# Performance work log

Hardware: AMD Instinct MI355X
Metric: run time of the kernel (lower is better)

The kernel has to match this reference:

```python
import jax, jax.numpy as jnp
import numpy as np

CONV_DIMS = (-3, -2)   # spatial dims (channel-last layout)
RADIUS = (3, 3)        # window = 1 + 2*r = 7 per dim -> 49 cells
STEP = (1, 1)


def _unfold(x, dim, window, step):
    """torch.Tensor.unfold: dim -> out_len, window appended as last axis."""
    dim = dim % x.ndim
    n = x.shape[dim]
    starts = jnp.arange((n - window) // step + 1) * step          # [L]
    idx = starts[:, None] + jnp.arange(window)[None, :]           # [L, w]
    y = jnp.take(x, idx, axis=dim)                                # dim -> [L, w]
    return jnp.moveaxis(y, dim + 1, -1)                           # window axis to last


def _local_attention(x):
    # Unfold each conv dim; move its window axis to the front (as in the torch code).
    for i, r, s in zip(CONV_DIMS, RADIUS, STEP):
        x = _unfold(x, i, 1 + 2 * r, s)
        x = jnp.moveaxis(x, -1, 0)
    n_win = len(CONV_DIMS)
    cells = int(np.prod(x.shape[:n_win]))
    x = x.reshape((cells,) + x.shape[n_win:])      # [cells, B, H', W', C]
    center = cells // 2                            # spatial center of the window
    q = jnp.moveaxis(x[center:center + 1], 0, -2)  # [B, H', W', 1, C]
    k = jnp.moveaxis(jnp.concatenate([x[:center], x[center + 1:]], axis=0), 0, -2)  # [B,H',W',cells-1,C]
    d = q.shape[-1]
    scores = jnp.einsum('...qc,...kc->...qk', q, k) / jnp.sqrt(jnp.asarray(d, q.dtype))
    w = jax.nn.softmax(scores, axis=-1)
    out = jnp.einsum('...qk,...kc->...qc', w, k)   # keys double as values
    return out.squeeze(-2)                          # [B, H', W', C]


def setup_inputs() -> dict:
    key = jax.random.key(0)
    X = jax.random.normal(key, (4, 64, 64, 256), dtype=jnp.float32)
    return {"X": X}


def reference(X):
    return _local_attention(X)
```

## Files before the change

### kernel.cpp

```cpp
#include <hip/hip_runtime.h>

#define B_   4
#define H_   64
#define W_   64
#define C_   256
#define HO_  58
#define WO_  58
#define TI_  29
#define TJ_  8
#define GRID (B_ * TI_ * TJ_)

typedef __attribute__((ext_vector_type(8))) short bf16x8;
typedef __attribute__((ext_vector_type(4))) float f32x4;

__device__ __forceinline__ void split2(float a, float b, unsigned& hi, unsigned& lo) {
    unsigned ua = __builtin_bit_cast(unsigned, a);
    unsigned ub = __builtin_bit_cast(unsigned, b);
    hi = (ua >> 16) | (ub & 0xFFFF0000u);
    float ra = a - __builtin_bit_cast(float, ua & 0xFFFF0000u);
    float rb = b - __builtin_bit_cast(float, ub & 0xFFFF0000u);
    lo = (__builtin_bit_cast(unsigned, ra) >> 16) |
         (__builtin_bit_cast(unsigned, rb) & 0xFFFF0000u);
}

__device__ __forceinline__ bf16x8 ldfrag(const short* arr, int row, int col, int rowBytes) {
    int byte = (row * rowBytes + col * 2) ^ ((row & 7) << 4);
    return *(const bf16x8*)((const char*)arr + byte);
}

__global__ __launch_bounds__(256, 3) void convnd_attn_kernel(const float* __restrict__ X,
                                                             float* __restrict__ out) {
    __shared__ __align__(16) short UVh[128 * 64];
    __shared__ __align__(16) short UVl[128 * 64];
    __shared__ __align__(16) short Wh[16 * 128];
    __shared__ __align__(16) short Wl[16 * 128];
    __shared__ __align__(16) float SQ[128 * 16];
    __shared__ float psum[256];
    __shared__ float rtot[16];
    short* Qhi = (short*)SQ;
    short* Qlo = Qhi + 16 * 64;
    float* S   = SQ;

    const int sp  = (blockIdx.x & 7) * 116 + (blockIdx.x >> 3);
    const int tj  = sp & 7;
    const int rst = sp >> 3;
    const int ti  = rst % TI_;
    const int b   = rst / TI_;
    const int i0  = ti * 2;
    const int j0  = (tj < 7) ? tj * 8 : 50;

    const int tid  = threadIdx.x;
    const int wave = tid >> 6;
    const int lane = tid & 63;
    const int lr   = lane & 15;
    const int kb8  = (lane >> 4) << 3;

    const float* base = X + (size_t)b * (H_ * W_ * C_);

    f32x4 accS0 = {0.f, 0.f, 0.f, 0.f};
    f32x4 accS1 = {0.f, 0.f, 0.f, 0.f};

    const int ucell = tid >> 1;
    const int uhalf = (tid & 1) << 5;
    const int ur = ucell >> 4, uc = ucell & 15;
    const int ucol = min(j0 + uc, 63);
    const float* usrc0 = base + (((i0 + ur) * W_) + ucol) * C_ + uhalf;
    const int urb = ucell * 128 + uhalf * 2;
    const int usw = (ucell & 7) << 4;

    const int qpx = tid >> 4;
    const int qc4 = (tid & 15) << 2;
    const int qa = qpx >> 3, qb = qpx & 7;
    const float* qsrc0 = base + (((i0 + qa + 3) * W_) + (j0 + qb + 3)) * C_ + qc4;
    const int qrb = qpx * 128 + qc4 * 2;
    const int qsw = (qpx & 7) << 4;

    #pragma unroll
    for (int kc = 0; kc < 4; ++kc) {
        {
            const float* src = usrc0 + kc * 64;
            float4 xx[8];
            #pragma unroll
            for (int e = 0; e < 8; ++e) xx[e] = *(const float4*)(src + e * 4);
            #pragma unroll
            for (int g = 0; g < 4; ++g) {
                uint4 hi, lo;
                split2(xx[g*2].x,   xx[g*2].y,   hi.x, lo.x);
                split2(xx[g*2].z,   xx[g*2].w,   hi.y, lo.y);
                split2(xx[g*2+1].x, xx[g*2+1].y, hi.z, lo.z);
                split2(xx[g*2+1].z, xx[g*2+1].w, hi.w, lo.w);
                *(uint4*)((char*)UVh + ((urb + g * 16) ^ usw)) = hi;
                *(uint4*)((char*)UVl + ((urb + g * 16) ^ usw)) = lo;
            }
        }
        {
            float4 qx = *(const float4*)(qsrc0 + kc * 64);
            qx.x *= 0.0625f; qx.y *= 0.0625f; qx.z *= 0.0625f; qx.w *= 0.0625f;
            unsigned h0, l0, h1, l1;
            split2(qx.x, qx.y, h0, l0);
            split2(qx.z, qx.w, h1, l1);
            *(uint2*)((char*)Qhi + (qrb ^ qsw)) = make_uint2(h0, h1);
            *(uint2*)((char*)Qlo + (qrb ^ qsw)) = make_uint2(l0, l1);
        }
        __syncthreads();

        #pragma unroll
        for (int ks = 0; ks < 2; ++ks) {
            const int kcol = ks * 32 + kb8;
            bf16x8 qh = ldfrag(Qhi, lr, kcol, 128);
            bf16x8 ql = ldfrag(Qlo, lr, kcol, 128);
            {
                const int crow = (wave * 2 + 0) * 16 + lr;
                bf16x8 uh = ldfrag(UVh, crow, kcol, 128);
                bf16x8 ul = ldfrag(UVl, crow, kcol, 128);
                accS0 = __builtin_amdgcn_mfma_f32_16x16x32_bf16(uh, qh, accS0, 0, 0, 0);
                accS0 = __builtin_amdgcn_mfma_f32_16x16x32_bf16(uh, ql, accS0, 0, 0, 0);
                accS0 = __builtin_amdgcn_mfma_f32_16x16x32_bf16(ul, qh, accS0, 0, 0, 0);
            }
            {
                const int crow = (wave * 2 + 1) * 16 + lr;
                bf16x8 uh = ldfrag(UVh, crow, kcol, 128);
                bf16x8 ul = ldfrag(UVl, crow, kcol, 128);
                accS1 = __builtin_amdgcn_mfma_f32_16x16x32_bf16(uh, qh, accS1, 0, 0, 0);
                accS1 = __builtin_amdgcn_mfma_f32_16x16x32_bf16(uh, ql, accS1, 0, 0, 0);
                accS1 = __builtin_amdgcn_mfma_f32_16x16x32_bf16(ul, qh, accS1, 0, 0, 0);
            }
        }
        __syncthreads();
    }

    {
        const int mrow = (lane >> 4) << 2;
        #pragma unroll
        for (int rr = 0; rr < 4; ++rr) {
            S[((wave * 2 + 0) * 16 + mrow + rr) * 16 + lr] = accS0[rr];
            S[((wave * 2 + 1) * 16 + mrow + rr) * 16 + lr] = accS1[rr];
        }
    }
    __syncthreads();

    const int spx = tid & 15, seg = tid >> 4;
    {
        const int sa = spx >> 3, sb = spx & 7;
        float e[8]; float ps = 0.f;
        #pragma unroll
        for (int k = 0; k < 8; ++k) {
            const int cell = seg * 8 + k;
            const int cr = cell >> 4, cc = cell & 15;
            const int di = cr - sa, dj = cc - sb;
            const bool valid = (di >= 0) & (di <= 6) & (dj >= 0) & (dj <= 6)
                               & !((di == 3) & (dj == 3));
            e[k] = valid ? __expf(S[cell * 16 + spx]) : 0.f;
            ps += e[k];
        }
        psum[seg * 16 + spx] = ps;
        __syncthreads();
        if (tid < 16) {
            float t = 0.f;
            #pragma unroll
            for (int s2 = 0; s2 < 16; ++s2) t += psum[s2 * 16 + tid];
            rtot[tid] = 1.0f / t;
        }
        __syncthreads();
        const float rt = rtot[spx];
        unsigned h0,h1,h2,h3, l0,l1,l2,l3;
        split2(e[0]*rt, e[1]*rt, h0, l0);
        split2(e[2]*rt, e[3]*rt, h1, l1);
        split2(e[4]*rt, e[5]*rt, h2, l2);
        split2(e[6]*rt, e[7]*rt, h3, l3);
        const int wb = (spx * 256 + seg * 16) ^ ((spx & 7) << 4);
        *(uint4*)((char*)Wh + wb) = make_uint4(h0, h1, h2, h3);
        *(uint4*)((char*)Wl + wb) = make_uint4(l0, l1, l2, l3);
    }
    __syncthreads();

    const int cp  = tid & 63;
    const int chg = (tid >> 6) << 4;
    const int vr = (cp * 2) >> 4, vc = (cp * 2) & 15;
    const int vcol0 = min(j0 + vc, 63);
    const int vcol1 = min(j0 + vc + 1, 63);
    const float* vsrc0 = base + (((i0 + vr) * W_) + vcol0) * C_ + chg;
    const float* vsrc1 = base + (((i0 + vr) * W_) + vcol1) * C_ + chg;

    #pragma unroll
    for (int nc = 0; nc < 4; ++nc) {
        {
            float4 y0[4], y1[4];
            #pragma unroll
            for (int e = 0; e < 4; ++e) {
                y0[e] = *(const float4*)(vsrc0 + nc * 64 + e * 4);
                y1[e] = *(const float4*)(vsrc1 + nc * 64 + e * 4);
            }
            #pragma unroll
            for (int jj = 0; jj < 4; ++jj) {
                const int chb = chg + jj * 4;
                unsigned h, l;
                split2(y0[jj].x, y1[jj].x, h, l);
                { int by = ((chb+0) * 256 + cp * 4) ^ (((chb+0) & 7) << 4);
                  *(unsigned*)((char*)UVh + by) = h; *(unsigned*)((char*)UVl + by) = l; }
                split2(y0[jj].y, y1[jj].y, h, l);
                { int by = ((chb+1) * 256 + cp * 4) ^ (((chb+1) & 7) << 4);
                  *(unsigned*)((char*)UVh + by) = h; *(unsigned*)((char*)UVl + by) = l; }
                split2(y0[jj].z, y1[jj].z, h, l);
                { int by = ((chb+2) * 256 + cp * 4) ^ (((chb+2) & 7) << 4);
                  *(unsigned*)((char*)UVh + by) = h; *(unsigned*)((char*)UVl + by) = l; }
                split2(y0[jj].w, y1[jj].w, h, l);
                { int by = ((chb+3) * 256 + cp * 4) ^ (((chb+3) & 7) << 4);
                  *(unsigned*)((char*)UVh + by) = h; *(unsigned*)((char*)UVl + by) = l; }
            }
        }
        __syncthreads();

        f32x4 accO = {0.f, 0.f, 0.f, 0.f};
        #pragma unroll
        for (int ks = 0; ks < 4; ++ks) {
            const int kcol = ks * 32 + kb8;
            bf16x8 wh = ldfrag(Wh, lr, kcol, 256);
            bf16x8 wl = ldfrag(Wl, lr, kcol, 256);
            bf16x8 vh = ldfrag(UVh, wave * 16 + lr, kcol, 256);
            bf16x8 vl = ldfrag(UVl, wave * 16 + lr, kcol, 256);
            accO = __builtin_amdgcn_mfma_f32_16x16x32_bf16(wh, vh, accO, 0, 0, 0);
            accO = __builtin_amdgcn_mfma_f32_16x16x32_bf16(wh, vl, accO, 0, 0, 0);
            accO = __builtin_amdgcn_mfma_f32_16x16x32_bf16(wl, vh, accO, 0, 0, 0);
        }
        {
            const int ch = nc * 64 + wave * 16 + lr;
            const int mrow = (lane >> 4) << 2;
            #pragma unroll
            for (int rr = 0; rr < 4; ++rr) {
                const int px = mrow + rr;
                const int a = px >> 3, bb = px & 7;
                out[(((size_t)b * HO_ + (i0 + a)) * WO_ + (j0 + bb)) * C_ + ch] = accO[rr];
            }
        }
        __syncthreads();
    }
}

extern "C" void kernel_launch(void* const* d_in, const int* in_sizes, int n_in,
                              void* d_out, int out_size, void* d_ws, size_t ws_size,
                              hipStream_t stream) {
    const float* X = (const float*)d_in[0];
    float* outp    = (float*)d_out;
    hipLaunchKernelGGL(convnd_attn_kernel,
                       dim3(GRID), dim3(256), 0, stream, X, outp);
}
```

Measured before the change: 102.5 us.

## Load MFMA fragments directly from global memory, bypassing LDS staging

Builds the Q, U and V bf16 hi/lo fragments straight from global loads into registers instead of staging them through shared memory. The score phase gives each wave its own quarter of the channel dimension and writes per-wave partial score tiles, which the softmax step sums, so the per-chunk barriers go away. The output phase reads V with strided scalar global loads per lane and keeps the softmax weight fragments in registers. This removes LDS traffic and most __syncthreads, in exchange for uncoalesced scalar loads in the PV phase, more registers and a larger partial-score buffer in LDS.

```diff
diff --git a/kernel.cpp b/kernel.cpp
--- a/kernel.cpp
+++ b/kernel.cpp
@@ -23,6 +23,16 @@
          (__builtin_bit_cast(unsigned, rb) & 0xFFFF0000u);
 }
 
+__device__ __forceinline__ void split8(const float* v, bf16x8& h, bf16x8& l) {
+    uint4 hu, lu;
+    split2(v[0], v[1], hu.x, lu.x);
+    split2(v[2], v[3], hu.y, lu.y);
+    split2(v[4], v[5], hu.z, lu.z);
+    split2(v[6], v[7], hu.w, lu.w);
+    h = __builtin_bit_cast(bf16x8, hu);
+    l = __builtin_bit_cast(bf16x8, lu);
+}
+
 __device__ __forceinline__ bf16x8 ldfrag(const short* arr, int row, int col, int rowBytes) {
     int byte = (row * rowBytes + col * 2) ^ ((row & 7) << 4);
     return *(const bf16x8*)((const char*)arr + byte);
@@ -30,16 +40,11 @@
 
 __global__ __launch_bounds__(256, 3) void convnd_attn_kernel(const float* __restrict__ X,
                                                              float* __restrict__ out) {
-    __shared__ __align__(16) short UVh[128 * 64];
-    __shared__ __align__(16) short UVl[128 * 64];
+    __shared__ __align__(16) float Spart[4][128][16];
     __shared__ __align__(16) short Wh[16 * 128];
     __shared__ __align__(16) short Wl[16 * 128];
-    __shared__ __align__(16) float SQ[128 * 16];
-    __shared__ float psum[256];
+    __shared__ float psum[16][16];
     __shared__ float rtot[16];
-    short* Qhi = (short*)SQ;
-    short* Qlo = Qhi + 16 * 64;
-    float* S   = SQ;
 
     const int sp  = (blockIdx.x & 7) * 116 + (blockIdx.x >> 3);
     const int tj  = sp & 7;
@@ -53,89 +58,55 @@
     const int wave = tid >> 6;
     const int lane = tid & 63;
     const int lr   = lane & 15;
-    const int kb8  = (lane >> 4) << 3;
+    const int g    = lane >> 4;
+    const int kb8  = g << 3;
 
     const float* base = X + (size_t)b * (H_ * W_ * C_);
 
-    f32x4 accS0 = {0.f, 0.f, 0.f, 0.f};
-    f32x4 accS1 = {0.f, 0.f, 0.f, 0.f};
-
-    const int ucell = tid >> 1;
-    const int uhalf = (tid & 1) << 5;
-    const int ur = ucell >> 4, uc = ucell & 15;
-    const int ucol = min(j0 + uc, 63);
-    const float* usrc0 = base + (((i0 + ur) * W_) + ucol) * C_ + uhalf;
-    const int urb = ucell * 128 + uhalf * 2;
-    const int usw = (ucell & 7) << 4;
-
-    const int qpx = tid >> 4;
-    const int qc4 = (tid & 15) << 2;
-    const int qa = qpx >> 3, qb = qpx & 7;
-    const float* qsrc0 = base + (((i0 + qa + 3) * W_) + (j0 + qb + 3)) * C_ + qc4;
-    const int qrb = qpx * 128 + qc4 * 2;
-    const int qsw = (qpx & 7) << 4;
-
-    #pragma unroll
-    for (int kc = 0; kc < 4; ++kc) {
-        {
-            const float* src = usrc0 + kc * 64;
-            float4 xx[8];
-            #pragma unroll
-            for (int e = 0; e < 8; ++e) xx[e] = *(const float4*)(src + e * 4);
-            #pragma unroll
-            for (int g = 0; g < 4; ++g) {
-                uint4 hi, lo;
-                split2(xx[g*2].x,   xx[g*2].y,   hi.x, lo.x);
-                split2(xx[g*2].z,   xx[g*2].w,   hi.y, lo.y);
-                split2(xx[g*2+1].x, xx[g*2+1].y, hi.z, lo.z);
-                split2(xx[g*2+1].z, xx[g*2+1].w, hi.w, lo.w);
-                *(uint4*)((char*)UVh + ((urb + g * 16) ^ usw)) = hi;
-                *(uint4*)((char*)UVl + ((urb + g * 16) ^ usw)) = lo;
-            }
-        }
-        {
-            float4 qx = *(const float4*)(qsrc0 + kc * 64);
-            qx.x *= 0.0625f; qx.y *= 0.0625f; qx.z *= 0.0625f; qx.w *= 0.0625f;
-            unsigned h0, l0, h1, l1;
-            split2(qx.x, qx.y, h0, l0);
-            split2(qx.z, qx.w, h1, l1);
-            *(uint2*)((char*)Qhi + (qrb ^ qsw)) = make_uint2(h0, h1);
-            *(uint2*)((char*)Qlo + (qrb ^ qsw)) = make_uint2(l0, l1);
-        }
-        __syncthreads();
-
+    bf16x8 qh[2], ql[2];
+    {
+        const int aq = lr >> 3, bq = lr & 7;
+        const float* qp = base + (((i0 + aq + 3) * W_) + (j0 + bq + 3)) * C_
+                        + wave * 64 + kb8;
         #pragma unroll
         for (int ks = 0; ks < 2; ++ks) {
-            const int kcol = ks * 32 + kb8;
-            bf16x8 qh = ldfrag(Qhi, lr, kcol, 128);
-            bf16x8 ql = ldfrag(Qlo, lr, kcol, 128);
-            {
-                const int crow = (wave * 2 + 0) * 16 + lr;
-                bf16x8 uh = ldfrag(UVh, crow, kcol, 128);
-                bf16x8 ul = ldfrag(UVl, crow, kcol, 128);
-                accS0 = __builtin_amdgcn_mfma_f32_16x16x32_bf16(uh, qh, accS0, 0, 0, 0);
-                accS0 = __builtin_amdgcn_mfma_f32_16x16x32_bf16(uh, ql, accS0, 0, 0, 0);
-                accS0 = __builtin_amdgcn_mfma_f32_16x16x32_bf16(ul, qh, accS0, 0, 0, 0);
-            }
-            {
-                const int crow = (wave * 2 + 1) * 16 + lr;
-                bf16x8 uh = ldfrag(UVh, crow, kcol, 128);
-                bf16x8 ul = ldfrag(UVl, crow, kcol, 128);
-                accS1 = __builtin_amdgcn_mfma_f32_16x16x32_bf16(uh, qh, accS1, 0, 0, 0);
-                accS1 = __builtin_amdgcn_mfma_f32_16x16x32_bf16(uh, ql, accS1, 0, 0, 0);
-                accS1 = __builtin_amdgcn_mfma_f32_16x16x32_bf16(ul, qh, accS1, 0, 0, 0);
-            }
+            float v[8];
+            float4 x0 = *(const float4*)(qp + ks * 32);
+            float4 x1 = *(const float4*)(qp + ks * 32 + 4);
+            v[0]=x0.x*0.0625f; v[1]=x0.y*0.0625f; v[2]=x0.z*0.0625f; v[3]=x0.w*0.0625f;
+            v[4]=x1.x*0.0625f; v[5]=x1.y*0.0625f; v[6]=x1.z*0.0625f; v[7]=x1.w*0.0625f;
+            split8(v, qh[ks], ql[ks]);
         }
-        __syncthreads();
     }
 
-    {
-        const int mrow = (lane >> 4) << 2;
+    f32x4 accS[8];
+    #pragma unroll
+    for (int t = 0; t < 8; ++t) accS[t] = (f32x4){0.f, 0.f, 0.f, 0.f};
+
+    const int dj13 = (lr < 13) ? lr : 13;
+    const float* up0 = base + (j0 + dj13) * C_ + wave * 64 + kb8;
+    #pragma unroll
+    for (int t = 0; t < 8; ++t) {
+        const float* ur = up0 + (size_t)(i0 + t) * (W_ * C_);
         #pragma unroll
-        for (int rr = 0; rr < 4; ++rr) {
-            S[((wave * 2 + 0) * 16 + mrow + rr) * 16 + lr] = accS0[rr];
-            S[((wave * 2 + 1) * 16 + mrow + rr) * 16 + lr] = accS1[rr];
+        for (int ks = 0; ks < 2; ++ks) {
+            float v[8];
+            float4 x0 = *(const float4*)(ur + ks * 32);
+            float4 x1 = *(const float4*)(ur + ks * 32 + 4);
+            v[0]=x0.x; v[1]=x0.y; v[2]=x0.z; v[3]=x0.w;
+            v[4]=x1.x; v[5]=x1.y; v[6]=x1.z; v[7]=x1.w;
+            bf16x8 uh, ul;
+            split8(v, uh, ul);
+            accS[t] = __builtin_amdgcn_mfma_f32_16x16x32_bf16(uh, qh[ks], accS[t], 0, 0, 0);
+            accS[t] = __builtin_amdgcn_mfma_f32_16x16x32_bf16(uh, ql[ks], accS[t], 0, 0, 0);
+            accS[t] = __builtin_amdgcn_mfma_f32_16x16x32_bf16(ul, qh[ks], accS[t], 0, 0, 0);
         }
+    }
+    #pragma unroll
+    for (int t = 0; t < 8; ++t) {
+        #pragma unroll
+        for (int rr = 0; rr < 4; ++rr)
+            Spart[wave][t * 16 + g * 4 + rr][lr] = accS[t][rr];
     }
     __syncthreads();
 
@@ -146,20 +117,21 @@
         #pragma unroll
         for (int k = 0; k < 8; ++k) {
             const int cell = seg * 8 + k;
-            const int cr = cell >> 4, cc = cell & 15;
-            const int di = cr - sa, dj = cc - sb;
+            const int di = (cell >> 4) - sa, dj = (cell & 15) - sb;
             const bool valid = (di >= 0) & (di <= 6) & (dj >= 0) & (dj <= 6)
                                & !((di == 3) & (dj == 3));
-            e[k] = valid ? __expf(S[cell * 16 + spx]) : 0.f;
+            const float s = Spart[0][cell][spx] + Spart[1][cell][spx]
+                          + Spart[2][cell][spx] + Spart[3][cell][spx];
+            e[k] = valid ? __expf(s) : 0.f;
             ps += e[k];
         }
-        psum[seg * 16 + spx] = ps;
+        psum[seg][spx] = ps;
         __syncthreads();
         if (tid < 16) {
-            float t = 0.f;
+            float t2 = 0.f;
             #pragma unroll
-            for (int s2 = 0; s2 < 16; ++s2) t += psum[s2 * 16 + tid];
-            rtot[tid] = 1.0f / t;
+            for (int s2 = 0; s2 < 16; ++s2) t2 += psum[s2][tid];
+            rtot[tid] = 1.0f / t2;
         }
         __syncthreads();
         const float rt = rtot[spx];
@@ -174,66 +146,40 @@
     }
     __syncthreads();
 
-    const int cp  = tid & 63;
-    const int chg = (tid >> 6) << 4;
-    const int vr = (cp * 2) >> 4, vc = (cp * 2) & 15;
-    const int vcol0 = min(j0 + vc, 63);
-    const int vcol1 = min(j0 + vc + 1, 63);
-    const float* vsrc0 = base + (((i0 + vr) * W_) + vcol0) * C_ + chg;
-    const float* vsrc1 = base + (((i0 + vr) * W_) + vcol1) * C_ + chg;
+    bf16x8 wfh[4], wfl[4];
+    #pragma unroll
+    for (int ks = 0; ks < 4; ++ks) {
+        wfh[ks] = ldfrag(Wh, lr, ks * 32 + kb8, 256);
+        wfl[ks] = ldfrag(Wl, lr, ks * 32 + kb8, 256);
+    }
 
     #pragma unroll
-    for (int nc = 0; nc < 4; ++nc) {
-        {
-            float4 y0[4], y1[4];
-            #pragma unroll
-            for (int e = 0; e < 4; ++e) {
-                y0[e] = *(const float4*)(vsrc0 + nc * 64 + e * 4);
-                y1[e] = *(const float4*)(vsrc1 + nc * 64 + e * 4);
-            }
-            #pragma unroll
-            for (int jj = 0; jj < 4; ++jj) {
-                const int chb = chg + jj * 4;
-                unsigned h, l;
-                split2(y0[jj].x, y1[jj].x, h, l);
-                { int by = ((chb+0) * 256 + cp * 4) ^ (((chb+0) & 7) << 4);
-                  *(unsigned*)((char*)UVh + by) = h; *(unsigned*)((char*)UVl + by) = l; }
-                split2(y0[jj].y, y1[jj].y, h, l);
-                { int by = ((chb+1) * 256 + cp * 4) ^ (((chb+1) & 7) << 4);
-                  *(unsigned*)((char*)UVh + by) = h; *(unsigned*)((char*)UVl + by) = l; }
-                split2(y0[jj].z, y1[jj].z, h, l);
-                { int by = ((chb+2) * 256 + cp * 4) ^ (((chb+2) & 7) << 4);
-                  *(unsigned*)((char*)UVh + by) = h; *(unsigned*)((char*)UVl + by) = l; }
-                split2(y0[jj].w, y1[jj].w, h, l);
-                { int by = ((chb+3) * 256 + cp * 4) ^ (((chb+3) & 7) << 4);
-                  *(unsigned*)((char*)UVh + by) = h; *(unsigned*)((char*)UVl + by) = l; }
-            }
-        }
-        __syncthreads();
-
+    for (int cc = 0; cc < 4; ++cc) {
+        const int ch = (wave * 4 + cc) * 16 + lr;
         f32x4 accO = {0.f, 0.f, 0.f, 0.f};
         #pragma unroll
         for (int ks = 0; ks < 4; ++ks) {
-            const int kcol = ks * 32 + kb8;
-            bf16x8 wh = ldfrag(Wh, lr, kcol, 256);
-            bf16x8 wl = ldfrag(Wl, lr, kcol, 256);
-            bf16x8 vh = ldfrag(UVh, wave * 16 + lr, kcol, 256);
-            bf16x8 vl = ldfrag(UVl, wave * 16 + lr, kcol, 256);
-            accO = __builtin_amdgcn_mfma_f32_16x16x32_bf16(wh, vh, accO, 0, 0, 0);
-            accO = __builtin_amdgcn_mfma_f32_16x16x32_bf16(wh, vl, accO, 0, 0, 0);
-            accO = __builtin_amdgcn_mfma_f32_16x16x32_bf16(wl, vh, accO, 0, 0, 0);
+            const int di  = ks * 2 + (g >> 1);
+            const int dj0 = (g & 1) * 8;
+            const float* vb = base + (((i0 + di) * W_) + j0) * C_ + ch;
+            float v[8];
+            #pragma unroll
+            for (int e2 = 0; e2 < 8; ++e2) {
+                const int dj = (dj0 + e2 < 13) ? dj0 + e2 : 13;
+                v[e2] = vb[dj * C_];
+            }
+            bf16x8 vh, vl;
+            split8(v, vh, vl);
+            accO = __builtin_amdgcn_mfma_f32_16x16x32_bf16(wfh[ks], vh, accO, 0, 0, 0);
+            accO = __builtin_amdgcn_mfma_f32_16x16x32_bf16(wfh[ks], vl, accO, 0, 0, 0);
+            accO = __builtin_amdgcn_mfma_f32_16x16x32_bf16(wfl[ks], vh, accO, 0, 0, 0);
         }
-        {
-            const int ch = nc * 64 + wave * 16 + lr;
-            const int mrow = (lane >> 4) << 2;
-            #pragma unroll
-            for (int rr = 0; rr < 4; ++rr) {
-                const int px = mrow + rr;
-                const int a = px >> 3, bb = px & 7;
-                out[(((size_t)b * HO_ + (i0 + a)) * WO_ + (j0 + bb)) * C_ + ch] = accO[rr];
-            }
+        #pragma unroll
+        for (int rr = 0; rr < 4; ++rr) {
+            const int px = g * 4 + rr;
+            const int aa = px >> 3, bb = px & 7;
+            out[(((size_t)b * HO_ + (i0 + aa)) * WO_ + (j0 + bb)) * C_ + ch] = accO[rr];
         }
-        __syncthreads();
     }
 }
 
```

Result: faster. 91.64 us (-10.6%).
